# Kernel tuning notes

Hardware: AMD Instinct MI355X
Metric: run time of the kernel (lower is better)

The kernel has to match this reference:

```python
import jax, jax.numpy as jnp
import numpy as np

EPS = 1e-5

def setup_inputs() -> dict:
    key = jax.random.key(0)
    ks = jax.random.split(key, 10)
    B, C, H, W, D = 1, 128, 20, 20, 20
    Cq = C // 8
    s = 0.05
    return {
        "x":   jax.random.normal(ks[0], (B, C, H, W, D), jnp.float32),
        "wq":  jax.random.normal(ks[1], (Cq, C), jnp.float32) * s,
        "bq":  jnp.zeros((Cq,), jnp.float32),
        "wk":  jax.random.normal(ks[2], (Cq, C), jnp.float32) * s,
        "bk":  jnp.zeros((Cq,), jnp.float32),
        "wv":  jax.random.normal(ks[3], (C, C), jnp.float32) * s,
        "bv":  jnp.zeros((C,), jnp.float32),
        "wa":  jax.random.normal(ks[4], (C, C), jnp.float32) * s,
        "ba":  jnp.zeros((C,), jnp.float32),
        "bn_w": jnp.ones((C,), jnp.float32),
        "bn_b": jnp.zeros((C,), jnp.float32),
    }

def reference(x, wq, bq, wk, bk, wv, bv, wa, ba, bn_w, bn_b):
    B, C, H, W, D = x.shape
    N = H * W * D
    xf = x.reshape(B, C, N)                                   # (B,C,N)
    # 1x1 conv projections = per-position channel matmuls
    q = jnp.einsum('oc,bcn->bno', wq, xf) + bq                # (B,N,Cq)
    k = jnp.einsum('oc,bcn->bon', wk, xf) + bk[:, None]       # (B,Cq,N)
    v = jnp.einsum('oc,bcn->bon', wv, xf) + bv[:, None]       # (B,C,N)
    # raw (unscaled) attention, softmax over key positions
    att = jax.nn.softmax(jnp.einsum('bnc,bcm->bnm', q, k), axis=-1)  # (B,N,N)
    # att_value[b,c,i] = sum_j value[b,c,j] * att[b,i,j]
    av = jnp.einsum('bcj,bij->bci', v, att)                   # (B,C,N)
    y = jnp.einsum('oc,bcn->bon', wa, av) + ba[:, None]       # (B,C,N)
    # BatchNorm (training mode): per-channel stats over batch + spatial
    mean = jnp.mean(y, axis=(0, 2), keepdims=True)
    var = jnp.var(y, axis=(0, 2), keepdims=True)
    y = (y - mean) * jax.lax.rsqrt(var + EPS) * bn_w[:, None] + bn_b[:, None]
    out = jax.nn.relu(y) + xf
    return out.reshape(B, C, H, W, D)
```

## Files before the change

kernel.cpp:

```cpp
#include <hip/hip_runtime.h>
#include <math.h>

#define N_POS 8000
#define C_CH  128
#define KSPLIT 5
#define KT_PER 25

typedef __bf16 bf16x8 __attribute__((ext_vector_type(8)));
typedef float  f32x4  __attribute__((ext_vector_type(4)));

#define MFMA(a,b,c) __builtin_amdgcn_mfma_f32_16x16x32_bf16((a),(b),(c),0,0,0)


#define GLOAD_LDS(gp, lp) \
    __builtin_amdgcn_global_load_lds( \
        (const __attribute__((address_space(1))) void*)(gp), \
        (__attribute__((address_space(3))) void*)(lp), 16, 0, 0)

__global__ __launch_bounds__(256) void qkv_kernel(
    const float* __restrict__ x,
    const float* __restrict__ wq, const float* __restrict__ bq,
    const float* __restrict__ wk, const float* __restrict__ bk,
    const float* __restrict__ wv, const float* __restrict__ bv,
    __bf16* __restrict__ q_bf, __bf16* __restrict__ k_bf, __bf16* __restrict__ v_bf)
{
    __shared__ __bf16 x_lds[32 * 136];
    __shared__ __bf16 v_out[128 * 36];

    const int t    = threadIdx.x;
    const int n0   = blockIdx.x * 32;
    const int lane = t & 63;
    const int w    = t >> 6;
    const int l15  = lane & 15;
    const int quad = lane >> 4;

    for (int r = 0; r < 4; ++r) {
        int f = r * 256 + t;
        int ch = f >> 3, n4 = f & 7;
        float4 xv = *reinterpret_cast<const float4*>(&x[ch * N_POS + n0 + n4 * 4]);
        x_lds[(n4 * 4 + 0) * 136 + ch] = (__bf16)xv.x;
        x_lds[(n4 * 4 + 1) * 136 + ch] = (__bf16)xv.y;
        x_lds[(n4 * 4 + 2) * 136 + ch] = (__bf16)xv.z;
        x_lds[(n4 * 4 + 3) * 136 + ch] = (__bf16)xv.w;
    }

    bf16x8 aw[3][4];
    f32x4  acc[3][2];
    const int nmt = (w < 2) ? 3 : 2;
    for (int mi = 0; mi < nmt; ++mi) {
        int mt = w + 4 * mi;
        const float *wrow, *brow;
        if (mt == 0)      { wrow = wq + l15 * 128;               brow = bq; }
        else if (mt == 1) { wrow = wk + l15 * 128;               brow = bk; }
        else              { wrow = wv + ((mt - 2) * 16 + l15) * 128;
                            brow = bv + (mt - 2) * 16; }
        for (int ks = 0; ks < 4; ++ks) {
            float4 f0 = *reinterpret_cast<const float4*>(wrow + ks * 32 + quad * 8);
            float4 f1 = *reinterpret_cast<const float4*>(wrow + ks * 32 + quad * 8 + 4);
            bf16x8 a;
            a[0]=(__bf16)f0.x; a[1]=(__bf16)f0.y; a[2]=(__bf16)f0.z; a[3]=(__bf16)f0.w;
            a[4]=(__bf16)f1.x; a[5]=(__bf16)f1.y; a[6]=(__bf16)f1.z; a[7]=(__bf16)f1.w;
            aw[mi][ks] = a;
        }
        for (int ni = 0; ni < 2; ++ni) {
            acc[mi][ni][0] = brow[quad * 4 + 0]; acc[mi][ni][1] = brow[quad * 4 + 1];
            acc[mi][ni][2] = brow[quad * 4 + 2]; acc[mi][ni][3] = brow[quad * 4 + 3];
        }
    }
    __syncthreads();

    for (int ks = 0; ks < 4; ++ks) {
        bf16x8 b0 = *reinterpret_cast<const bf16x8*>(&x_lds[(0  + l15) * 136 + ks * 32 + quad * 8]);
        bf16x8 b1 = *reinterpret_cast<const bf16x8*>(&x_lds[(16 + l15) * 136 + ks * 32 + quad * 8]);
        for (int mi = 0; mi < nmt; ++mi) {
            acc[mi][0] = MFMA(aw[mi][ks], b0, acc[mi][0]);
            acc[mi][1] = MFMA(aw[mi][ks], b1, acc[mi][1]);
        }
    }

    union S4 { short4 s; __bf16 b[4]; };
    for (int mi = 0; mi < nmt; ++mi) {
        int mt = w + 4 * mi;
        for (int ni = 0; ni < 2; ++ni) {
            S4 u;
            u.b[0]=(__bf16)acc[mi][ni][0]; u.b[1]=(__bf16)acc[mi][ni][1];
            u.b[2]=(__bf16)acc[mi][ni][2]; u.b[3]=(__bf16)acc[mi][ni][3];
            int n = n0 + ni * 16 + l15;
            if (mt == 0) {
                *reinterpret_cast<short4*>(&q_bf[n * 16 + quad * 4]) = u.s;
            } else if (mt == 1) {
                *reinterpret_cast<short4*>(&k_bf[n * 16 + quad * 4]) = u.s;
            } else {
                int ch0 = (mt - 2) * 16 + quad * 4;
                int nl  = ni * 16 + l15;
                v_out[(ch0 + 0) * 36 + nl] = u.b[0];
                v_out[(ch0 + 1) * 36 + nl] = u.b[1];
                v_out[(ch0 + 2) * 36 + nl] = u.b[2];
                v_out[(ch0 + 3) * 36 + nl] = u.b[3];
            }
        }
    }
    __syncthreads();
    for (int r = 0; r < 4; ++r) {
        int f = r * 256 + t;
        int ch = f >> 3, n4 = f & 7;
        int2 d = *reinterpret_cast<const int2*>(&v_out[ch * 36 + n4 * 4]);
        *reinterpret_cast<int2*>(&v_bf[ch * N_POS + n0 + n4 * 4]) = d;
    }
}

__global__ __launch_bounds__(256, 4) void attn_kernel(
    const __bf16* __restrict__ q_bf, const __bf16* __restrict__ k_bf,
    const __bf16* __restrict__ v_bf, float* __restrict__ av_part,
    float* __restrict__ l_part)
{
    __shared__ __bf16 v_buf[2][8192];
    __shared__ __bf16 k_buf[2][1024];
    __shared__ __bf16 p_lds[2048];

    const int t    = threadIdx.x;
    const int qt   = blockIdx.x % 250;
    const int sp   = blockIdx.x / 250;
    const int n0q  = qt * 32;
    const int lane = t & 63;
    const int w    = t >> 6;
    const int l15  = lane & 15;
    const int quad = lane >> 4;

    const int chL   = lane >> 3;
    const int vpart = (lane & 7) ^ chL;
    const int kkey  = lane >> 1;
    const int khalf = lane & 1;

    bf16x8 aq[2];
    for (int ni = 0; ni < 2; ++ni) {
        for (int j = 0; j < 8; ++j) aq[ni][j] = (__bf16)0.0f;
        if (quad < 2)
            aq[ni] = *reinterpret_cast<const bf16x8*>(
                &q_bf[(n0q + ni * 16 + l15) * 16 + quad * 8]);
    }
    bf16x8 ones;
    for (int j = 0; j < 8; ++j) ones[j] = (__bf16)1.0f;

    f32x4 acc[2][2];
    for (int mi = 0; mi < 2; ++mi)
        for (int ni = 0; ni < 2; ++ni)
            for (int r = 0; r < 4; ++r) acc[mi][ni][r] = 0.f;
    f32x4 lacc[2];
    for (int ni = 0; ni < 2; ++ni)
        for (int r = 0; r < 4; ++r) lacc[ni][r] = 0.f;

    const int kt0 = kt0 < 0 ? 0 : sp * KT_PER;

    auto stage = [&](int kt, int buf) {
        const int n0k = kt * 64;
        for (int r = 0; r < 4; ++r) {
            int R = w * 4 + r;
            GLOAD_LDS(v_bf + (8 * R + chL) * N_POS + n0k + vpart * 8,
                      &v_buf[buf][R * 512]);
        }
        for (int h = 0; h < 2; ++h) {
            GLOAD_LDS(k_bf + (size_t)(n0k + h * 32 + kkey) * 16 + khalf * 8,
                      &k_buf[buf][h * 512]);
        }
    };

    stage(kt0, 0);

    const int oS  = w * 2 + (quad >> 1);
    const int sub = (quad & 1) * 4;

    for (int kt = kt0; kt < kt0 + KT_PER; ++kt) {
        const int cur = (kt - kt0) & 1;
        __syncthreads();

        bf16x8 ak;
        for (int j = 0; j < 8; ++j) ak[j] = (__bf16)0.0f;
        if (quad < 2)
            ak = *reinterpret_cast<const bf16x8*>(
                &k_buf[cur][(w * 16 + l15) * 16 + quad * 8]);
        f32x4 s0, s1;
        for (int r = 0; r < 4; ++r) { s0[r] = 0.f; s1[r] = 0.f; }
        s0 = MFMA(ak, aq[0], s0);
        s1 = MFMA(ak, aq[1], s1);
        union S4 { short4 sh; __bf16 b[4]; };
        {
            S4 u;
            u.b[0] = (__bf16)__expf(s0[0]); u.b[1] = (__bf16)__expf(s0[1]);
            u.b[2] = (__bf16)__expf(s0[2]); u.b[3] = (__bf16)__expf(s0[3]);
            *reinterpret_cast<short4*>(&p_lds[(oS * 32 + l15) * 8 + sub]) = u.sh;
            u.b[0] = (__bf16)__expf(s1[0]); u.b[1] = (__bf16)__expf(s1[1]);
            u.b[2] = (__bf16)__expf(s1[2]); u.b[3] = (__bf16)__expf(s1[3]);
            *reinterpret_cast<short4*>(&p_lds[(oS * 32 + 16 + l15) * 8 + sub]) = u.sh;
        }
        __syncthreads();

        if (kt + 1 < kt0 + KT_PER) stage(kt + 1, cur ^ 1);

        const int chl = l15 & 7;
        for (int ks = 0; ks < 2; ++ks) {
            int pz = ((ks * 4 + quad) ^ chl);
            bf16x8 a0 = *reinterpret_cast<const bf16x8*>(
                &v_buf[cur][(((2 * w)     * 2 + (l15 >> 3)) * 64 + chl * 8 + pz) * 8]);
            bf16x8 a1 = *reinterpret_cast<const bf16x8*>(
                &v_buf[cur][(((2 * w + 1) * 2 + (l15 >> 3)) * 64 + chl * 8 + pz) * 8]);
            bf16x8 p0 = *reinterpret_cast<const bf16x8*>(
                &p_lds[((ks * 4 + quad) * 32 + 0  + l15) * 8]);
            bf16x8 p1 = *reinterpret_cast<const bf16x8*>(
                &p_lds[((ks * 4 + quad) * 32 + 16 + l15) * 8]);
            acc[0][0] = MFMA(a0, p0, acc[0][0]);
            acc[0][1] = MFMA(a0, p1, acc[0][1]);
            acc[1][0] = MFMA(a1, p0, acc[1][0]);
            acc[1][1] = MFMA(a1, p1, acc[1][1]);
            if (w == 0) {
                lacc[0] = MFMA(ones, p0, lacc[0]);
                lacc[1] = MFMA(ones, p1, lacc[1]);
            }
        }
    }

    float* dst = av_part + (size_t)sp * 1024000;
    for (int mi = 0; mi < 2; ++mi)
        for (int ni = 0; ni < 2; ++ni) {
            int n  = n0q + ni * 16 + l15;
            int ch = (2 * w + mi) * 16 + quad * 4;
            *reinterpret_cast<f32x4*>(&dst[n * 128 + ch]) = acc[mi][ni];
        }
    if (w == 0 && quad == 0) {
        l_part[sp * N_POS + n0q + 0  + l15] = lacc[0][0];
        l_part[sp * N_POS + n0q + 16 + l15] = lacc[1][0];
    }
}

__global__ __launch_bounds__(256) void proj_out_kernel(
    const float* __restrict__ av_part, const float* __restrict__ l_part,
    const float* __restrict__ wa, const float* __restrict__ ba,
    float* __restrict__ y_ws, float* __restrict__ bn_sum, float* __restrict__ bn_sumsq)
{
    __shared__ __bf16 b_lds[4096];

    const int t    = threadIdx.x;
    const int n0   = blockIdx.x * 32;
    const int lane = t & 63;
    const int w    = t >> 6;
    const int l15  = lane & 15;
    const int quad = lane >> 4;

    for (int r = 0; r < 2; ++r) {
        int g = r * 256 + t;
        int n = g >> 4, oc = g & 15;
        float l = 0.f;
#pragma unroll
        for (int s = 0; s < KSPLIT; ++s) l += l_part[s * N_POS + n0 + n];
        float4 a0 = make_float4(0.f, 0.f, 0.f, 0.f);
        float4 a1 = make_float4(0.f, 0.f, 0.f, 0.f);
#pragma unroll
        for (int s = 0; s < KSPLIT; ++s) {
            const float* p = av_part + (size_t)s * 1024000 + (n0 + n) * 128 + oc * 8;
            float4 u = *reinterpret_cast<const float4*>(p);
            float4 v = *reinterpret_cast<const float4*>(p + 4);
            a0.x += u.x; a0.y += u.y; a0.z += u.z; a0.w += u.w;
            a1.x += v.x; a1.y += v.y; a1.z += v.z; a1.w += v.w;
        }
        float inv = 1.f / l;
        union { int4 iv; __bf16 b[8]; } u;
        u.b[0]=(__bf16)(a0.x*inv); u.b[1]=(__bf16)(a0.y*inv);
        u.b[2]=(__bf16)(a0.z*inv); u.b[3]=(__bf16)(a0.w*inv);
        u.b[4]=(__bf16)(a1.x*inv); u.b[5]=(__bf16)(a1.y*inv);
        u.b[6]=(__bf16)(a1.z*inv); u.b[7]=(__bf16)(a1.w*inv);
        int A = (n >> 4) * 16 + oc;
        int slot = (n & 15) ^ (oc & 7);
        *reinterpret_cast<int4*>(&b_lds[(A * 16 + slot) * 8]) = u.iv;
    }

    bf16x8 aw[2][4];
    f32x4  acc[2][2];
    for (int mi = 0; mi < 2; ++mi) {
        int mt = 2 * w + mi;
        const float* wrow = wa + (mt * 16 + l15) * 128;
        for (int ks = 0; ks < 4; ++ks) {
            float4 f0 = *reinterpret_cast<const float4*>(wrow + ks * 32 + quad * 8);
            float4 f1 = *reinterpret_cast<const float4*>(wrow + ks * 32 + quad * 8 + 4);
            bf16x8 a;
            a[0]=(__bf16)f0.x; a[1]=(__bf16)f0.y; a[2]=(__bf16)f0.z; a[3]=(__bf16)f0.w;
            a[4]=(__bf16)f1.x; a[5]=(__bf16)f1.y; a[6]=(__bf16)f1.z; a[7]=(__bf16)f1.w;
            aw[mi][ks] = a;
        }
        for (int ni = 0; ni < 2; ++ni) {
            acc[mi][ni][0] = ba[mt * 16 + quad * 4 + 0];
            acc[mi][ni][1] = ba[mt * 16 + quad * 4 + 1];
            acc[mi][ni][2] = ba[mt * 16 + quad * 4 + 2];
            acc[mi][ni][3] = ba[mt * 16 + quad * 4 + 3];
        }
    }
    __syncthreads();

    for (int ks = 0; ks < 4; ++ks) {
        int oc = ks * 4 + quad;
        int slot = l15 ^ (oc & 7);
        bf16x8 b0 = *reinterpret_cast<const bf16x8*>(&b_lds[((0  + oc) * 16 + slot) * 8]);
        bf16x8 b1 = *reinterpret_cast<const bf16x8*>(&b_lds[((16 + oc) * 16 + slot) * 8]);
        for (int mi = 0; mi < 2; ++mi) {
            acc[mi][0] = MFMA(aw[mi][ks], b0, acc[mi][0]);
            acc[mi][1] = MFMA(aw[mi][ks], b1, acc[mi][1]);
        }
    }

    for (int mi = 0; mi < 2; ++mi) {
        for (int r = 0; r < 4; ++r) {
            int ch = (2 * w + mi) * 16 + quad * 4 + r;
            float v0 = acc[mi][0][r];
            float v1 = acc[mi][1][r];
            y_ws[ch * N_POS + n0 + 0  + l15] = v0;
            y_ws[ch * N_POS + n0 + 16 + l15] = v1;
            float s1 = v0 + v1;
            float s2 = v0 * v0 + v1 * v1;
#pragma unroll
            for (int off = 8; off >= 1; off >>= 1) {
                s1 += __shfl_xor(s1, off, 64);
                s2 += __shfl_xor(s2, off, 64);
            }
            if (l15 == 0) {
                atomicAdd(&bn_sum[ch],   s1);
                atomicAdd(&bn_sumsq[ch], s2);
            }
        }
    }
}

__global__ __launch_bounds__(256) void bn_relu_kernel(
    const float* __restrict__ y_ws, const float* __restrict__ x,
    const float* __restrict__ bn_sum, const float* __restrict__ bn_sumsq,
    const float* __restrict__ bn_w, const float* __restrict__ bn_b,
    float* __restrict__ out)
{
    const int i4 = blockIdx.x * 256 + threadIdx.x;
    const int c  = i4 / 2000;
    const float mean  = bn_sum[c]   * (1.f / 8000.f);
    const float var   = bn_sumsq[c] * (1.f / 8000.f) - mean * mean;
    const float rstd  = rsqrtf(var + 1e-5f);
    const float scale = bn_w[c] * rstd;
    const float shift = bn_b[c] - mean * scale;

    float4 y4 = reinterpret_cast<const float4*>(y_ws)[i4];
    float4 x4 = reinterpret_cast<const float4*>(x)[i4];
    float4 o4;
    o4.x = fmaxf(y4.x * scale + shift, 0.f) + x4.x;
    o4.y = fmaxf(y4.y * scale + shift, 0.f) + x4.y;
    o4.z = fmaxf(y4.z * scale + shift, 0.f) + x4.z;
    o4.w = fmaxf(y4.w * scale + shift, 0.f) + x4.w;
    reinterpret_cast<float4*>(out)[i4] = o4;
}

extern "C" void kernel_launch(void* const* d_in, const int* in_sizes, int n_in,
                              void* d_out, int out_size, void* d_ws, size_t ws_size,
                              hipStream_t stream)
{
    const float* x    = (const float*)d_in[0];
    const float* wq   = (const float*)d_in[1];
    const float* bq   = (const float*)d_in[2];
    const float* wk   = (const float*)d_in[3];
    const float* bk   = (const float*)d_in[4];
    const float* wv   = (const float*)d_in[5];
    const float* bv   = (const float*)d_in[6];
    const float* wa   = (const float*)d_in[7];
    const float* ba   = (const float*)d_in[8];
    const float* bn_w = (const float*)d_in[9];
    const float* bn_b = (const float*)d_in[10];
    float* out = (float*)d_out;

    char* base = (char*)d_ws;
    float*  av_part = (float*)base;
    __bf16* q_bf    = (__bf16*)(base + 20480000);
    __bf16* k_bf    = (__bf16*)(base + 20736000);
    __bf16* v_bf    = (__bf16*)(base + 20992000);
    float*  l_part  = (float*)(base + 23040000);
    float*  bn_sum   = (float*)(base + 23200000);
    float*  bn_sumsq = bn_sum + 128;
    float*  y_ws    = (float*)(base + 23201024);

    hipMemsetAsync(bn_sum, 0, 1024, stream);
    qkv_kernel<<<250, 256, 0, stream>>>(x, wq, bq, wk, bk, wv, bv, q_bf, k_bf, v_bf);
    attn_kernel<<<250 * KSPLIT, 256, 0, stream>>>(q_bf, k_bf, v_bf, av_part, l_part);
    proj_out_kernel<<<250, 256, 0, stream>>>(av_part, l_part, wa, ba, y_ws, bn_sum, bn_sumsq);
    bn_relu_kernel<<<1000, 256, 0, stream>>>(y_ws, x, bn_sum, bn_sumsq, bn_w, bn_b, out);
}
```

Before: 179.3 us.

## Widen attention query tile to 64 and prefetch next K/V before score compute

Each attention block now handles 64 query positions instead of 32, halving the number of blocks and reusing each staged V/K tile for twice as many queries. The next tile's prefetch is issued right after the first barrier instead of after the probability write. The second __syncthreads is replaced by an explicit lgkmcnt wait plus raw barrier. The row-sum MFMA is spread across all waves instead of only wave 0. This raises register and LDS use, so occupancy is lowered via launch bounds, which risks less latency hiding and fewer blocks to fill the GPU.

Measured after the change: 161.2 us. -10.1%, faster.

```diff
diff --git a/kernel.cpp b/kernel.cpp
--- a/kernel.cpp
+++ b/kernel.cpp
@@ -5,6 +5,7 @@
 #define C_CH  128
 #define KSPLIT 5
 #define KT_PER 25
+#define QTILES 125
 
 typedef __bf16 bf16x8 __attribute__((ext_vector_type(8)));
 typedef float  f32x4  __attribute__((ext_vector_type(4)));
@@ -109,19 +110,19 @@
     }
 }
 
-__global__ __launch_bounds__(256, 4) void attn_kernel(
+__global__ __launch_bounds__(256, 3) void attn_kernel(
     const __bf16* __restrict__ q_bf, const __bf16* __restrict__ k_bf,
     const __bf16* __restrict__ v_bf, float* __restrict__ av_part,
     float* __restrict__ l_part)
 {
     __shared__ __bf16 v_buf[2][8192];
     __shared__ __bf16 k_buf[2][1024];
-    __shared__ __bf16 p_lds[2048];
+    __shared__ __bf16 p_lds[4096];
 
     const int t    = threadIdx.x;
-    const int qt   = blockIdx.x % 250;
-    const int sp   = blockIdx.x / 250;
-    const int n0q  = qt * 32;
+    const int qt   = blockIdx.x % QTILES;
+    const int sp   = blockIdx.x / QTILES;
+    const int n0q  = qt * 64;
     const int lane = t & 63;
     const int w    = t >> 6;
     const int l15  = lane & 15;
@@ -132,8 +133,8 @@
     const int kkey  = lane >> 1;
     const int khalf = lane & 1;
 
-    bf16x8 aq[2];
-    for (int ni = 0; ni < 2; ++ni) {
+    bf16x8 aq[4];
+    for (int ni = 0; ni < 4; ++ni) {
         for (int j = 0; j < 8; ++j) aq[ni][j] = (__bf16)0.0f;
         if (quad < 2)
             aq[ni] = *reinterpret_cast<const bf16x8*>(
@@ -142,15 +143,14 @@
     bf16x8 ones;
     for (int j = 0; j < 8; ++j) ones[j] = (__bf16)1.0f;
 
-    f32x4 acc[2][2];
+    f32x4 acc[2][4];
     for (int mi = 0; mi < 2; ++mi)
-        for (int ni = 0; ni < 2; ++ni)
+        for (int ni = 0; ni < 4; ++ni)
             for (int r = 0; r < 4; ++r) acc[mi][ni][r] = 0.f;
-    f32x4 lacc[2];
-    for (int ni = 0; ni < 2; ++ni)
-        for (int r = 0; r < 4; ++r) lacc[ni][r] = 0.f;
-
-    const int kt0 = kt0 < 0 ? 0 : sp * KT_PER;
+    f32x4 lacc;
+    for (int r = 0; r < 4; ++r) lacc[r] = 0.f;
+
+    const int kt0 = sp * KT_PER;
 
     auto stage = [&](int kt, int buf) {
         const int n0k = kt * 64;
@@ -159,77 +159,81 @@
             GLOAD_LDS(v_bf + (8 * R + chL) * N_POS + n0k + vpart * 8,
                       &v_buf[buf][R * 512]);
         }
-        for (int h = 0; h < 2; ++h) {
-            GLOAD_LDS(k_bf + (size_t)(n0k + h * 32 + kkey) * 16 + khalf * 8,
-                      &k_buf[buf][h * 512]);
-        }
+        if (w < 2)
+            GLOAD_LDS(k_bf + (size_t)(n0k + w * 32 + kkey) * 16 + khalf * 8,
+                      &k_buf[buf][w * 512]);
     };
 
     stage(kt0, 0);
 
     const int oS  = w * 2 + (quad >> 1);
     const int sub = (quad & 1) * 4;
+
+    union S4 { short4 sh; __bf16 b[4]; };
 
     for (int kt = kt0; kt < kt0 + KT_PER; ++kt) {
         const int cur = (kt - kt0) & 1;
         __syncthreads();
+
+        if (kt + 1 < kt0 + KT_PER) stage(kt + 1, cur ^ 1);
 
         bf16x8 ak;
         for (int j = 0; j < 8; ++j) ak[j] = (__bf16)0.0f;
         if (quad < 2)
             ak = *reinterpret_cast<const bf16x8*>(
                 &k_buf[cur][(w * 16 + l15) * 16 + quad * 8]);
-        f32x4 s0, s1;
-        for (int r = 0; r < 4; ++r) { s0[r] = 0.f; s1[r] = 0.f; }
-        s0 = MFMA(ak, aq[0], s0);
-        s1 = MFMA(ak, aq[1], s1);
-        union S4 { short4 sh; __bf16 b[4]; };
-        {
+#pragma unroll
+        for (int ni = 0; ni < 4; ++ni) {
+            f32x4 s;
+            for (int r = 0; r < 4; ++r) s[r] = 0.f;
+            s = MFMA(ak, aq[ni], s);
             S4 u;
-            u.b[0] = (__bf16)__expf(s0[0]); u.b[1] = (__bf16)__expf(s0[1]);
-            u.b[2] = (__bf16)__expf(s0[2]); u.b[3] = (__bf16)__expf(s0[3]);
-            *reinterpret_cast<short4*>(&p_lds[(oS * 32 + l15) * 8 + sub]) = u.sh;
-            u.b[0] = (__bf16)__expf(s1[0]); u.b[1] = (__bf16)__expf(s1[1]);
-            u.b[2] = (__bf16)__expf(s1[2]); u.b[3] = (__bf16)__expf(s1[3]);
-            *reinterpret_cast<short4*>(&p_lds[(oS * 32 + 16 + l15) * 8 + sub]) = u.sh;
-        }
-        __syncthreads();
-
-        if (kt + 1 < kt0 + KT_PER) stage(kt + 1, cur ^ 1);
+            u.b[0] = (__bf16)__expf(s[0]); u.b[1] = (__bf16)__expf(s[1]);
+            u.b[2] = (__bf16)__expf(s[2]); u.b[3] = (__bf16)__expf(s[3]);
+            *reinterpret_cast<short4*>(
+                &p_lds[(oS * 64 + ni * 16 + l15) * 8 + sub]) = u.sh;
+        }
+
+        asm volatile("s_waitcnt lgkmcnt(0)" ::: "memory");
+        __builtin_amdgcn_s_barrier();
+        asm volatile("" ::: "memory");
+        __builtin_amdgcn_sched_barrier(0);
 
         const int chl = l15 & 7;
+#pragma unroll
         for (int ks = 0; ks < 2; ++ks) {
             int pz = ((ks * 4 + quad) ^ chl);
             bf16x8 a0 = *reinterpret_cast<const bf16x8*>(
                 &v_buf[cur][(((2 * w)     * 2 + (l15 >> 3)) * 64 + chl * 8 + pz) * 8]);
             bf16x8 a1 = *reinterpret_cast<const bf16x8*>(
                 &v_buf[cur][(((2 * w + 1) * 2 + (l15 >> 3)) * 64 + chl * 8 + pz) * 8]);
-            bf16x8 p0 = *reinterpret_cast<const bf16x8*>(
-                &p_lds[((ks * 4 + quad) * 32 + 0  + l15) * 8]);
-            bf16x8 p1 = *reinterpret_cast<const bf16x8*>(
-                &p_lds[((ks * 4 + quad) * 32 + 16 + l15) * 8]);
+            const int ob = (ks * 4 + quad) * 64;
+            bf16x8 p0 = *reinterpret_cast<const bf16x8*>(&p_lds[(ob +  0 + l15) * 8]);
+            bf16x8 p1 = *reinterpret_cast<const bf16x8*>(&p_lds[(ob + 16 + l15) * 8]);
+            bf16x8 p2 = *reinterpret_cast<const bf16x8*>(&p_lds[(ob + 32 + l15) * 8]);
+            bf16x8 p3 = *reinterpret_cast<const bf16x8*>(&p_lds[(ob + 48 + l15) * 8]);
             acc[0][0] = MFMA(a0, p0, acc[0][0]);
             acc[0][1] = MFMA(a0, p1, acc[0][1]);
+            acc[0][2] = MFMA(a0, p2, acc[0][2]);
+            acc[0][3] = MFMA(a0, p3, acc[0][3]);
             acc[1][0] = MFMA(a1, p0, acc[1][0]);
             acc[1][1] = MFMA(a1, p1, acc[1][1]);
-            if (w == 0) {
-                lacc[0] = MFMA(ones, p0, lacc[0]);
-                lacc[1] = MFMA(ones, p1, lacc[1]);
-            }
+            acc[1][2] = MFMA(a1, p2, acc[1][2]);
+            acc[1][3] = MFMA(a1, p3, acc[1][3]);
+            bf16x8 pw = *reinterpret_cast<const bf16x8*>(&p_lds[(ob + w * 16 + l15) * 8]);
+            lacc = MFMA(ones, pw, lacc);
         }
     }
 
     float* dst = av_part + (size_t)sp * 1024000;
     for (int mi = 0; mi < 2; ++mi)
-        for (int ni = 0; ni < 2; ++ni) {
+        for (int ni = 0; ni < 4; ++ni) {
             int n  = n0q + ni * 16 + l15;
             int ch = (2 * w + mi) * 16 + quad * 4;
             *reinterpret_cast<f32x4*>(&dst[n * 128 + ch]) = acc[mi][ni];
         }
-    if (w == 0 && quad == 0) {
-        l_part[sp * N_POS + n0q + 0  + l15] = lacc[0][0];
-        l_part[sp * N_POS + n0q + 16 + l15] = lacc[1][0];
-    }
+    if (quad == 0)
+        l_part[sp * N_POS + n0q + w * 16 + l15] = lacc[0];
 }
 
 __global__ __launch_bounds__(256) void proj_out_kernel(
@@ -381,7 +385,7 @@
 
     hipMemsetAsync(bn_sum, 0, 1024, stream);
     qkv_kernel<<<250, 256, 0, stream>>>(x, wq, bq, wk, bk, wv, bv, q_bf, k_bf, v_bf);
-    attn_kernel<<<250 * KSPLIT, 256, 0, stream>>>(q_bf, k_bf, v_bf, av_part, l_part);
+    attn_kernel<<<QTILES * KSPLIT, 256, 0, stream>>>(q_bf, k_bf, v_bf, av_part, l_part);
     proj_out_kernel<<<250, 256, 0, stream>>>(av_part, l_part, wa, ba, y_ws, bn_sum, bn_sumsq);
     bn_relu_kernel<<<1000, 256, 0, stream>>>(y_ws, x, bn_sum, bn_sumsq, bn_w, bn_b, out);
 }
```
